# Kernel optimization log

Hardware: AMD Instinct MI355X
Metric: run time of the kernel (lower is better)

Reference implementation:

```python
import jax, jax.numpy as jnp
import numpy as np

IN_CH = 384
HEAD_DIM = 32
MAX_SEQ = 64          # P, tokens per window
N_HEADS = IN_CH // HEAD_DIM
PART = int(np.sqrt(MAX_SEQ))  # 8, window side
SCALE = HEAD_DIM ** -0.5


def _relative_position_index():
    # Swin relative position index, [P*P] int
    h = np.arange(PART)
    coords = np.stack(np.meshgrid(h, h, indexing='ij')).reshape(2, -1)  # [2, P]
    rel = coords[:, :, None] - coords[:, None, :]                        # [2, P, P]
    rel = rel.transpose(1, 2, 0).astype(np.int64)
    rel[:, :, 0] += PART - 1
    rel[:, :, 1] += PART - 1
    rel[:, :, 0] *= 2 * PART - 1
    return rel.sum(-1).reshape(-1)  # [P*P]

REL_IDX = jnp.asarray(_relative_position_index())


def setup_inputs() -> dict:
    key = jax.random.key(0)
    ks = jax.random.split(key, 6)
    B, G, P, D = 32, 64, MAX_SEQ, IN_CH
    x = jax.random.normal(ks[0], (B, G, P, D), dtype=jnp.float32)
    Wqkv = jax.random.normal(ks[1], (D, 3 * D), dtype=jnp.float32) * (D ** -0.5)
    bqkv = jnp.zeros((3 * D,), dtype=jnp.float32)
    Wm = jax.random.normal(ks[2], (D, D), dtype=jnp.float32) * (D ** -0.5)
    bm = jnp.zeros((D,), dtype=jnp.float32)
    # torch init is zeros; use small normal so bias actually affects the output
    rel_table = jax.random.normal(ks[3], ((2 * PART - 1) ** 2, N_HEADS), dtype=jnp.float32) * 0.02
    return {"x": x, "Wqkv": Wqkv, "bqkv": bqkv, "Wm": Wm, "bm": bm, "rel_table": rel_table}


def reference(x, Wqkv, bqkv, Wm, bm, rel_table):
    B, G, P, D = x.shape
    H, DH = N_HEADS, HEAD_DIM
    qkv = x @ Wqkv + bqkv                                   # [B,G,P,3D]
    q, k, v = jnp.split(qkv, 3, axis=-1)
    q = q.reshape(B, G, P, H, DH) * SCALE
    k = k.reshape(B, G, P, H, DH)
    v = v.reshape(B, G, P, H, DH)
    attn = jnp.einsum('bgihd,bgjhd->bghij', q, k)           # [B,G,H,P,P]
    bias = rel_table[REL_IDX].reshape(P, P, H).transpose(2, 0, 1)  # [H,P,P]
    attn = jax.nn.softmax(attn + bias[None, None], axis=-1)
    out = jnp.einsum('bghij,bgjhd->bgihd', attn, v)         # [B,G,P,H,DH]
    out = out.reshape(B, G, P, D)
    return out @ Wm + bm
```

## Files before the change

### kernel.cpp

```cpp
#include <hip/hip_runtime.h>
#include <stdint.h>


typedef __attribute__((ext_vector_type(4))) float f32x4;
typedef __attribute__((ext_vector_type(4))) short s16x4;
typedef __attribute__((ext_vector_type(8))) short s16x8;

#define DEVI static __device__ __forceinline__

DEVI unsigned short f2bf(float f) {
  union { float f; uint32_t u; } v; v.f = f;
  return (unsigned short)((v.u + 0x7FFFu + ((v.u >> 16) & 1u)) >> 16);
}

DEVI f32x4 zero4() { f32x4 z; z[0] = 0.f; z[1] = 0.f; z[2] = 0.f; z[3] = 0.f; return z; }

#if defined(__has_builtin)
#if __has_builtin(__builtin_amdgcn_mfma_f32_16x16x16bf16_1k)
#define MFMA16_BUILTIN 1
#endif
#if __has_builtin(__builtin_amdgcn_global_load_lds)
#define HAS_GLLDS 1
#endif
#endif

DEVI f32x4 mfma16(s16x4 a, s16x4 b, f32x4 c) {
#ifdef MFMA16_BUILTIN
  return __builtin_amdgcn_mfma_f32_16x16x16bf16_1k(a, b, c, 0, 0, 0);
#else
  asm volatile("v_mfma_f32_16x16x16_bf16 %0, %1, %2, %0" : "+v"(c) : "v"(a), "v"(b));
  return c;
#endif
}

DEVI f32x4 mfma32(s16x8 a, s16x8 b, f32x4 c) {
  return __builtin_amdgcn_mfma_f32_16x16x32_bf16(a, b, c, 0, 0, 0);
}

DEVI void stage1k(const unsigned short* g_lane, unsigned short* lds_base) {
#ifdef HAS_GLLDS
  __builtin_amdgcn_global_load_lds(
      (const __attribute__((address_space(1))) unsigned int*)g_lane,
      (__attribute__((address_space(3))) unsigned int*)lds_base, 16, 0, 0);
#else
  *(s16x8*)(lds_base + (threadIdx.x & 63) * 8) = *(const s16x8*)g_lane;
#endif
}

__global__ void prep_wqkvT(const float* __restrict__ W, unsigned short* __restrict__ WT) {
  int t = blockIdx.x * 256 + threadIdx.x;
  if (t >= 1152 * 384) return;
  int n = t / 384, k = t - n * 384;
  float s = (n < 384) ? 0.17677669529663687f : 1.0f;
  WT[t] = f2bf(W[(size_t)k * 1152 + n] * s);
}

__global__ void prep_wmT(const float* __restrict__ W, unsigned short* __restrict__ WT) {
  int t = blockIdx.x * 256 + threadIdx.x;
  if (t >= 384 * 384) return;
  int n = t / 384, k = t - n * 384;
  WT[t] = f2bf(W[(size_t)k * 384 + n]);
}

__global__ void prep_bqkv(const float* __restrict__ b, float* __restrict__ bs) {
  int t = blockIdx.x * 256 + threadIdx.x;
  if (t >= 1152) return;
  bs[t] = b[t] * ((t < 384) ? 0.17677669529663687f : 1.0f);
}

__global__ void prep_biasF(const float* __restrict__ rel, float* __restrict__ biasF) {
  int t = blockIdx.x * 256 + threadIdx.x;
  if (t >= 12288) return;
  int h = t >> 10;
  int r = (t >> 6) & 15;
  int lane = t & 63;
  int jt = r >> 2, it = r & 3;
  int lg = lane >> 4, lr = lane & 15;
  int i = it * 16 + lr;
#pragma unroll
  for (int e = 0; e < 4; ++e) {
    int j = jt * 16 + lg * 4 + e;
    int idx = ((i >> 3) - (j >> 3) + 7) * 15 + ((i & 7) - (j & 7) + 7);
    biasF[t * 4 + e] = rel[idx * 12 + h];
  }
}

__global__ void fill_val(float* o, int n, float v) {
  int t = blockIdx.x * 256 + threadIdx.x;
  if (t < n) o[t] = v;
}

__global__ __launch_bounds__(256) void conv_bf16(const float* __restrict__ x,
                                                 unsigned short* __restrict__ xb) {
  const size_t nchunk = 131072UL * 384 / 8;
  const size_t stride = (size_t)gridDim.x * blockDim.x;
  for (size_t i = (size_t)blockIdx.x * blockDim.x + threadIdx.x; i < nchunk; i += stride) {
    f32x4 a = *(const f32x4*)(x + i * 8);
    f32x4 b = *(const f32x4*)(x + i * 8 + 4);
    s16x8 p;
    p[0] = (short)f2bf(a[0]); p[1] = (short)f2bf(a[1]);
    p[2] = (short)f2bf(a[2]); p[3] = (short)f2bf(a[3]);
    p[4] = (short)f2bf(b[0]); p[5] = (short)f2bf(b[1]);
    p[6] = (short)f2bf(b[2]); p[7] = (short)f2bf(b[3]);
    *(s16x8*)(xb + i * 8) = p;
  }
}

template <bool QKV_EPI>
__global__ __launch_bounds__(512, 4) void gemm_k(const unsigned short* __restrict__ A,
                                                 const unsigned short* __restrict__ BT,
                                                 const float* __restrict__ bias,
                                                 void* __restrict__ Cv) {
  constexpr int K = 384;
  constexpr int NT = QKV_EPI ? 9 : 3;
  constexpr int N = NT * 128;
  __shared__ unsigned short sm[2][16384];
  const int bid = blockIdx.x;
  const int swz = (bid & 7) * (NT * 128) + (bid >> 3);
  const int n0 = (swz % NT) * 128;
  const int m0 = (swz / NT) * 128;
  const int tid = threadIdx.x;
  const int lane = tid & 63, wv = tid >> 6;
  const int wr = wv >> 2, wc = wv & 3;
  const int lg = lane >> 4, lr = lane & 15;

  const int scol = ((lane & 7) ^ (lane >> 3)) * 8;
  const unsigned short* Ag = A + (size_t)(m0 + wv * 16 + (lane >> 3)) * K + scol;
  const unsigned short* Bg = BT + (size_t)(n0 + wv * 16 + (lane >> 3)) * K + scol;

  f32x4 acc[4][2];
#pragma unroll
  for (int i = 0; i < 4; ++i)
#pragma unroll
    for (int j = 0; j < 2; ++j) acc[i][j] = zero4();

  auto STAGE = [&](int buf, int k0) {
#pragma unroll
    for (int c2 = 0; c2 < 2; ++c2)
      stage1k(Ag + (size_t)(c2 * 8) * K + k0, &sm[buf][(wv * 16 + c2 * 8) * 64]);
#pragma unroll
    for (int c2 = 0; c2 < 2; ++c2)
      stage1k(Bg + (size_t)(c2 * 8) * K + k0, &sm[buf][8192 + (wv * 16 + c2 * 8) * 64]);
  };
  const int sa = (lr & 7) << 3;
  auto COMPUTE = [&](int buf) {
#pragma unroll
    for (int kk = 0; kk < 64; kk += 32) {
      s16x8 af[4], bf[2];
#pragma unroll
      for (int mt = 0; mt < 4; ++mt)
        af[mt] = *(const s16x8*)&sm[buf][(wr * 64 + 16 * mt + lr) * 64 + ((kk + 8 * lg) ^ sa)];
#pragma unroll
      for (int nt = 0; nt < 2; ++nt)
        bf[nt] = *(const s16x8*)&sm[buf][8192 + (wc * 32 + 16 * nt + lr) * 64 + ((kk + 8 * lg) ^ sa)];
#pragma unroll
      for (int mt = 0; mt < 4; ++mt)
#pragma unroll
        for (int nt = 0; nt < 2; ++nt)
          acc[mt][nt] = mfma32(af[mt], bf[nt], acc[mt][nt]);
    }
  };

  STAGE(0, 0);
  __syncthreads();
  int cur = 0;
#pragma unroll 1
  for (int t = 0; t < 5; ++t) {
    STAGE(cur ^ 1, (t + 1) * 64);
    COMPUTE(cur);
    __syncthreads();
    cur ^= 1;
  }
  COMPUTE(cur);

  const int crow = m0 + wr * 64 + 4 * lg;
  const int ccol = n0 + wc * 32 + lr;
  if constexpr (QKV_EPI) {
    const int sel = n0 / 384;
    unsigned short* qkv = (unsigned short*)Cv;
    if (sel < 2) {
      unsigned short* tile = &sm[0][0];
#pragma unroll
      for (int nt = 0; nt < 2; ++nt) {
        const int cc = wc * 32 + 16 * nt + lr;
        const float bv = bias[n0 + cc];
#pragma unroll
        for (int mt = 0; mt < 4; ++mt) {
#pragma unroll
          for (int e = 0; e < 4; ++e) {
            const int r = wr * 64 + 16 * mt + 4 * lg + e;
            tile[r * 128 + (cc ^ ((r & 7) << 3))] = f2bf(acc[mt][nt][e] + bv);
          }
        }
      }
      __syncthreads();
      const int hbase = (n0 - sel * 384) >> 5;
      const int tr = wv * 16 + (lane >> 2);
      const int gtok = m0 + tr;
      const int w2 = gtok >> 6, t0r = gtok & 63;
#pragma unroll
      for (int hh = 0; hh < 4; ++hh) {
        const int chunk = hh * 4 + (lane & 3);
        s16x8 v = *(const s16x8*)&tile[tr * 128 + ((chunk * 8) ^ ((tr & 7) << 3))];
        unsigned short* dst = qkv + (((size_t)w2 * 12 + hbase + hh) * 3 + sel) * 2048 +
                              t0r * 32 + (lane & 3) * 8;
        *(s16x8*)dst = v;
      }
    } else {
      const int window = crow >> 6;
      const int t0 = crow & 63;
#pragma unroll
      for (int nt = 0; nt < 2; ++nt) {
        const int col = ccol + 16 * nt;
        const int hcol = col - 768;
        const int h = hcol >> 5, d = hcol & 31;
        const float bv = bias[col];
        unsigned short* base = qkv + (((size_t)window * 12 + h) * 3 + 2) * 2048;
#pragma unroll
        for (int mt = 0; mt < 4; ++mt) {
          s16x4 pk;
#pragma unroll
          for (int e = 0; e < 4; ++e) pk[e] = (short)f2bf(acc[mt][nt][e] + bv);
          *(s16x4*)&base[d * 64 + t0 + 16 * mt] = pk;
        }
      }
    }
  } else {
    float* C = (float*)Cv;
#pragma unroll
    for (int mt = 0; mt < 4; ++mt)
#pragma unroll
      for (int nt = 0; nt < 2; ++nt) {
        const int col = ccol + 16 * nt;
        const float bv = bias[col];
#pragma unroll
        for (int e = 0; e < 4; ++e)
          C[(size_t)(crow + 16 * mt + e) * N + col] = acc[mt][nt][e] + bv;
      }
  }
}

__global__ __launch_bounds__(256) void attn_k(const unsigned short* __restrict__ qkv,
                                              const float* __restrict__ biasF,
                                              unsigned short* __restrict__ attnout) {
  const int lane = threadIdx.x & 63;
  const int wv = threadIdx.x >> 6;
  const int wh = blockIdx.x * 4 + wv;
  const int window = wh / 12;
  const int h = wh - window * 12;
  const int lg = lane >> 4, lr = lane & 15;

  const unsigned short* hb = qkv + (size_t)wh * 6144;
  const unsigned short* Qh = hb;
  const unsigned short* Kh = hb + 2048;
  const unsigned short* Vth = hb + 4096;

  s16x8 ka[4], qb[4];
#pragma unroll
  for (int jt = 0; jt < 4; ++jt)
    ka[jt] = *(const s16x8*)&Kh[(jt * 16 + lr) * 32 + 8 * lg];
#pragma unroll
  for (int it = 0; it < 4; ++it)
    qb[it] = *(const s16x8*)&Qh[(it * 16 + lr) * 32 + 8 * lg];

  f32x4 c[4][4];
#pragma unroll
  for (int a = 0; a < 4; ++a)
#pragma unroll
    for (int b2 = 0; b2 < 4; ++b2) c[a][b2] = zero4();

#pragma unroll
  for (int jt = 0; jt < 4; ++jt)
#pragma unroll
    for (int it = 0; it < 4; ++it)
      c[jt][it] = mfma32(ka[jt], qb[it], c[jt][it]);

  const f32x4* bF = (const f32x4*)biasF + ((size_t)h * 16) * 64 + lane;
#pragma unroll
  for (int jt = 0; jt < 4; ++jt)
#pragma unroll
    for (int it = 0; it < 4; ++it)
      c[jt][it] += bF[(jt * 4 + it) * 64];

  s16x4 pb[4][4];
#pragma unroll
  for (int it = 0; it < 4; ++it) {
    float m = -3.0e38f;
#pragma unroll
    for (int jt = 0; jt < 4; ++jt)
#pragma unroll
      for (int e = 0; e < 4; ++e) m = fmaxf(m, c[jt][it][e]);
    m = fmaxf(m, __shfl_xor(m, 16));
    m = fmaxf(m, __shfl_xor(m, 32));
    float s = 0.f;
#pragma unroll
    for (int jt = 0; jt < 4; ++jt)
#pragma unroll
      for (int e = 0; e < 4; ++e) {
        float p = __expf(c[jt][it][e] - m);
        c[jt][it][e] = p;
        s += p;
      }
    s += __shfl_xor(s, 16);
    s += __shfl_xor(s, 32);
    const float inv = 1.f / s;
#pragma unroll
    for (int jt = 0; jt < 4; ++jt) {
      s16x4 pk;
#pragma unroll
      for (int e = 0; e < 4; ++e) pk[e] = (short)f2bf(c[jt][it][e] * inv);
      pb[jt][it] = pk;
    }
  }

  f32x4 o[2][4];
#pragma unroll
  for (int a = 0; a < 2; ++a)
#pragma unroll
    for (int b2 = 0; b2 < 4; ++b2) o[a][b2] = zero4();

#pragma unroll
  for (int jt = 0; jt < 4; ++jt) {
    s16x4 va[2];
#pragma unroll
    for (int dt = 0; dt < 2; ++dt)
      va[dt] = *(const s16x4*)&Vth[(dt * 16 + lr) * 64 + jt * 16 + 4 * lg];
#pragma unroll
    for (int dt = 0; dt < 2; ++dt)
#pragma unroll
      for (int it = 0; it < 4; ++it)
        o[dt][it] = mfma16(va[dt], pb[jt][it], o[dt][it]);
  }

  unsigned short* ob = attnout + (size_t)window * 64 * 384;
#pragma unroll
  for (int dt = 0; dt < 2; ++dt)
#pragma unroll
    for (int it = 0; it < 4; ++it) {
      s16x4 pk;
#pragma unroll
      for (int e = 0; e < 4; ++e) pk[e] = (short)f2bf(o[dt][it][e]);
      *(s16x4*)&ob[(size_t)(it * 16 + lr) * 384 + h * 32 + dt * 16 + 4 * lg] = pk;
    }
}

extern "C" void kernel_launch(void* const* d_in, const int* in_sizes, int n_in,
                              void* d_out, int out_size, void* d_ws, size_t ws_size,
                              hipStream_t stream) {
  const float* x = (const float*)d_in[0];
  const float* Wqkv = (const float*)d_in[1];
  const float* bqkv = (const float*)d_in[2];
  const float* Wm = (const float*)d_in[3];
  const float* bm = (const float*)d_in[4];
  const float* rel = (const float*)d_in[5];

  const size_t M = 131072;
  char* ws = (char*)d_ws;
  size_t off = 0;
  unsigned short* qkv = (unsigned short*)(ws + off);   off += M * 1152 * 2;
  unsigned short* xb = (unsigned short*)(ws + off);    off += M * 384 * 2;
  unsigned short* WqkvT = (unsigned short*)(ws + off); off += 1152 * 384 * 2;
  unsigned short* WmT = (unsigned short*)(ws + off);   off += 384 * 384 * 2;
  float* biasF = (float*)(ws + off);                   off += 12 * 16 * 64 * 4 * 4;
  float* bqkvs = (float*)(ws + off);                   off += 1152 * 4;
  unsigned short* attnout = xb;

  if (ws_size < off) {
    fill_val<<<(out_size + 255) / 256, 256, 0, stream>>>((float*)d_out, out_size, 12345.0f);
    return;
  }

  prep_wqkvT<<<(1152 * 384 + 255) / 256, 256, 0, stream>>>(Wqkv, WqkvT);
  prep_wmT<<<(384 * 384 + 255) / 256, 256, 0, stream>>>(Wm, WmT);
  prep_bqkv<<<5, 256, 0, stream>>>(bqkv, bqkvs);
  prep_biasF<<<48, 256, 0, stream>>>(rel, biasF);
  conv_bf16<<<2048, 256, 0, stream>>>(x, xb);

  gemm_k<true><<<9216, 512, 0, stream>>>(xb, WqkvT, bqkvs, qkv);
  attn_k<<<6144, 256, 0, stream>>>(qkv, biasF, attnout);
  gemm_k<false><<<3072, 512, 0, stream>>>(attnout, WmT, bm, d_out);
}
```

Before: 461.9 us.

## Fuse fp32-to-bf16 input conversion into QKV GEMM A-tile staging

Drops the standalone conversion kernel that wrote a bf16 copy of x. The QKV GEMM now loads fp32 A rows into registers, packs them to bf16 and writes them into swizzled LDS after the compute step, with the global load issued early for overlap. This removes one full read/write pass over the activations. In exchange, each of the nine N-tiles re-reads fp32 A, doubling A bytes per tile, and A staging moves from direct global-to-LDS loads to a register path. The workspace gets a dedicated attention-output buffer.

```diff
diff --git a/kernel.cpp b/kernel.cpp
--- a/kernel.cpp
+++ b/kernel.cpp
@@ -45,6 +45,15 @@
 #else
   *(s16x8*)(lds_base + (threadIdx.x & 63) * 8) = *(const s16x8*)g_lane;
 #endif
+}
+
+DEVI s16x8 pack8(f32x4 a, f32x4 b) {
+  s16x8 p;
+  p[0] = (short)f2bf(a[0]); p[1] = (short)f2bf(a[1]);
+  p[2] = (short)f2bf(a[2]); p[3] = (short)f2bf(a[3]);
+  p[4] = (short)f2bf(b[0]); p[5] = (short)f2bf(b[1]);
+  p[6] = (short)f2bf(b[2]); p[7] = (short)f2bf(b[3]);
+  return p;
 }
 
 __global__ void prep_wqkvT(const float* __restrict__ W, unsigned short* __restrict__ WT) {
@@ -90,24 +99,8 @@
   if (t < n) o[t] = v;
 }
 
-__global__ __launch_bounds__(256) void conv_bf16(const float* __restrict__ x,
-                                                 unsigned short* __restrict__ xb) {
-  const size_t nchunk = 131072UL * 384 / 8;
-  const size_t stride = (size_t)gridDim.x * blockDim.x;
-  for (size_t i = (size_t)blockIdx.x * blockDim.x + threadIdx.x; i < nchunk; i += stride) {
-    f32x4 a = *(const f32x4*)(x + i * 8);
-    f32x4 b = *(const f32x4*)(x + i * 8 + 4);
-    s16x8 p;
-    p[0] = (short)f2bf(a[0]); p[1] = (short)f2bf(a[1]);
-    p[2] = (short)f2bf(a[2]); p[3] = (short)f2bf(a[3]);
-    p[4] = (short)f2bf(b[0]); p[5] = (short)f2bf(b[1]);
-    p[6] = (short)f2bf(b[2]); p[7] = (short)f2bf(b[3]);
-    *(s16x8*)(xb + i * 8) = p;
-  }
-}
-
 template <bool QKV_EPI>
-__global__ __launch_bounds__(512, 4) void gemm_k(const unsigned short* __restrict__ A,
+__global__ __launch_bounds__(512, 4) void gemm_k(const void* __restrict__ Av,
                                                  const unsigned short* __restrict__ BT,
                                                  const float* __restrict__ bias,
                                                  void* __restrict__ Cv) {
@@ -125,8 +118,16 @@
   const int lg = lane >> 4, lr = lane & 15;
 
   const int scol = ((lane & 7) ^ (lane >> 3)) * 8;
-  const unsigned short* Ag = A + (size_t)(m0 + wv * 16 + (lane >> 3)) * K + scol;
   const unsigned short* Bg = BT + (size_t)(n0 + wv * 16 + (lane >> 3)) * K + scol;
+  const unsigned short* Ag16 =
+      QKV_EPI ? nullptr
+              : (const unsigned short*)Av + (size_t)(m0 + wv * 16 + (lane >> 3)) * K + scol;
+
+  const int ra = tid >> 2;
+  const int g0 = (tid & 3) * 2;
+  const float* Axg = QKV_EPI ? (const float*)Av + (size_t)(m0 + ra) * K + g0 * 8 : nullptr;
+  const int dsw0 = ra * 64 + (g0 ^ (ra & 7)) * 8;
+  const int dsw1 = ra * 64 + ((g0 + 1) ^ (ra & 7)) * 8;
 
   f32x4 acc[4][2];
 #pragma unroll
@@ -134,10 +135,28 @@
 #pragma unroll
     for (int j = 0; j < 2; ++j) acc[i][j] = zero4();
 
+  f32x4 a0, a1, a2, a3;
+  auto GLOADA = [&](int k0) {
+    if constexpr (QKV_EPI) {
+      const float* p = Axg + k0;
+      a0 = *(const f32x4*)p;
+      a1 = *(const f32x4*)(p + 4);
+      a2 = *(const f32x4*)(p + 8);
+      a3 = *(const f32x4*)(p + 12);
+    }
+  };
+  auto DSWA = [&](int buf) {
+    if constexpr (QKV_EPI) {
+      *(s16x8*)&sm[buf][dsw0] = pack8(a0, a1);
+      *(s16x8*)&sm[buf][dsw1] = pack8(a2, a3);
+    }
+  };
   auto STAGE = [&](int buf, int k0) {
-#pragma unroll
-    for (int c2 = 0; c2 < 2; ++c2)
-      stage1k(Ag + (size_t)(c2 * 8) * K + k0, &sm[buf][(wv * 16 + c2 * 8) * 64]);
+    if constexpr (!QKV_EPI) {
+#pragma unroll
+      for (int c2 = 0; c2 < 2; ++c2)
+        stage1k(Ag16 + (size_t)(c2 * 8) * K + k0, &sm[buf][(wv * 16 + c2 * 8) * 64]);
+    }
 #pragma unroll
     for (int c2 = 0; c2 < 2; ++c2)
       stage1k(Bg + (size_t)(c2 * 8) * K + k0, &sm[buf][8192 + (wv * 16 + c2 * 8) * 64]);
@@ -161,13 +180,17 @@
     }
   };
 
+  GLOADA(0);
   STAGE(0, 0);
+  DSWA(0);
   __syncthreads();
   int cur = 0;
 #pragma unroll 1
   for (int t = 0; t < 5; ++t) {
+    GLOADA((t + 1) * 64);
     STAGE(cur ^ 1, (t + 1) * 64);
     COMPUTE(cur);
+    DSWA(cur ^ 1);
     __syncthreads();
     cur ^= 1;
   }
@@ -357,13 +380,12 @@
   const size_t M = 131072;
   char* ws = (char*)d_ws;
   size_t off = 0;
-  unsigned short* qkv = (unsigned short*)(ws + off);   off += M * 1152 * 2;
-  unsigned short* xb = (unsigned short*)(ws + off);    off += M * 384 * 2;
-  unsigned short* WqkvT = (unsigned short*)(ws + off); off += 1152 * 384 * 2;
-  unsigned short* WmT = (unsigned short*)(ws + off);   off += 384 * 384 * 2;
-  float* biasF = (float*)(ws + off);                   off += 12 * 16 * 64 * 4 * 4;
-  float* bqkvs = (float*)(ws + off);                   off += 1152 * 4;
-  unsigned short* attnout = xb;
+  unsigned short* qkv = (unsigned short*)(ws + off);     off += M * 1152 * 2;
+  unsigned short* attnout = (unsigned short*)(ws + off); off += M * 384 * 2;
+  unsigned short* WqkvT = (unsigned short*)(ws + off);   off += 1152 * 384 * 2;
+  unsigned short* WmT = (unsigned short*)(ws + off);     off += 384 * 384 * 2;
+  float* biasF = (float*)(ws + off);                     off += 12 * 16 * 64 * 4 * 4;
+  float* bqkvs = (float*)(ws + off);                     off += 1152 * 4;
 
   if (ws_size < off) {
     fill_val<<<(out_size + 255) / 256, 256, 0, stream>>>((float*)d_out, out_size, 12345.0f);
@@ -374,9 +396,8 @@
   prep_wmT<<<(384 * 384 + 255) / 256, 256, 0, stream>>>(Wm, WmT);
   prep_bqkv<<<5, 256, 0, stream>>>(bqkv, bqkvs);
   prep_biasF<<<48, 256, 0, stream>>>(rel, biasF);
-  conv_bf16<<<2048, 256, 0, stream>>>(x, xb);
-
-  gemm_k<true><<<9216, 512, 0, stream>>>(xb, WqkvT, bqkvs, qkv);
+
+  gemm_k<true><<<9216, 512, 0, stream>>>(x, WqkvT, bqkvs, qkv);
   attn_k<<<6144, 256, 0, stream>>>(qkv, biasF, attnout);
   gemm_k<false><<<3072, 512, 0, stream>>>(attnout, WmT, bm, d_out);
 }
```

Measured after the change: 477.2 us. +3.3%, slower.
